# Optimization experiments

Measured on AMD Instinct MI355X. Metric: run time of the kernel, lower is better.

The kernel has to match this reference:

```python
import jax, jax.numpy as jnp
import numpy as np

SAME_RANGE = 1.0  # forward() default same_range
FLOW_SCALE = 32.0  # realistic pixel displacements


def setup_inputs() -> dict:
    key = jax.random.key(0)
    k1, k2, k3 = jax.random.split(key, 3)
    H, W, C = 2160, 3840, 3
    img = jax.random.uniform(k1, (H, W, C), dtype=jnp.float32)
    flow = jax.random.normal(k2, (H, W, 2), dtype=jnp.float32) * FLOW_SCALE
    depth = jax.random.uniform(k3, (H, W), dtype=jnp.float32) * 100.0 + 0.1
    return {"img": img, "flow": flow, "depth": depth}


def reference(img, flow, depth):
    """Forward warping with depth z-buffer occlusion resolution.

    Each source pixel (y,x) is scattered to p1 = p0 + flow (clamped to the
    image). At each target cell, only the contributions whose depth is within
    SAME_RANGE of the minimum arriving depth survive; surviving contributions
    are averaged. Empty cells stay zero (matches np.zeros_like init in the
    original C-library warp).
    """
    H, W, C = img.shape
    N = H * W
    gy, gx = jnp.meshgrid(jnp.arange(H, dtype=flow.dtype),
                          jnp.arange(W, dtype=flow.dtype), indexing='ij')
    # safe_x / safe_y clamped target coordinates
    tx = jnp.clip(gx + flow[..., 0], 0.0, W - 1)
    ty = jnp.clip(gy + flow[..., 1], 0.0, H - 1)
    ix = jnp.round(tx).astype(jnp.int32)
    iy = jnp.round(ty).astype(jnp.int32)
    idx = jax.lax.stop_gradient((iy * W + ix).reshape(N))  # [N] flat targets

    d = depth.reshape(N)
    # z-buffer: min depth landing at each target cell
    zmin = jnp.full((N,), jnp.inf, dtype=d.dtype).at[idx].min(d)
    keep = (d <= zmin[idx] + SAME_RANGE).astype(img.dtype)  # [N]

    src = img.reshape(N, C) * keep[:, None]
    num = jnp.zeros((N, C), dtype=img.dtype).at[idx].add(src)
    cnt = jnp.zeros((N,), dtype=img.dtype).at[idx].add(keep)
    out = jnp.where(cnt[:, None] > 0, num / jnp.maximum(cnt, 1.0)[:, None], 0.0)
    return out.reshape(H, W, C)
```

## Files before the change

### kernel.cpp

```cpp
#include <hip/hip_runtime.h>

#define HH 2160
#define WW 3840
#define NN (HH * WW)

#define SROWS 2
#define NSTRIP (HH / SROWS)
#define CPS (SROWS * WW)

#define BTH 256
#define GRP 2
#define GPX 4
#define PXB (BTH * GRP * GPX)

#define WIN 192

#define CSTRIDE 16

#define ICAP 12288
#define ECAP 262144
#define E0BASE ((u32)NSTRIP * ICAP)
#define E1BASE (E0BASE + ECAP)
#define TOTAL_RECS ((size_t)E1BASE + ECAP)

typedef unsigned long long u64;
typedef unsigned int u32;
typedef float f4n __attribute__((ext_vector_type(4)));

__device__ __forceinline__ u32 strip_base(int s) {
    if (s == 0) return E0BASE;
    if (s == NSTRIP - 1) return E1BASE;
    return (u32)s * ICAP;
}


__global__ __launch_bounds__(256) void init_cursor_kernel(u32* __restrict__ cursor)
{
    int s = blockIdx.x * blockDim.x + threadIdx.x;
    if (s < NSTRIP) cursor[(size_t)s * CSTRIDE] = strip_base(s);
}

__global__ __launch_bounds__(BTH, 6) void scatter_kernel(
    const float4* __restrict__ img4,
    const float4* __restrict__ flow4,
    const float4* __restrict__ depth4,
    u32* __restrict__ cursor,
    u64* __restrict__ recs)
{
    __shared__ u32 lc[WIN];
    __shared__ u32 gb[WIN];

    const int t = threadIdx.x;
    if (t < WIN) lc[t] = 0;
    __syncthreads();

    const int wb = blockIdx.x * PXB;
    const int ywb = wb / WW;
    int w0 = (ywb >> 1) - (WIN / 2);
    w0 = w0 < 0 ? 0 : (w0 > NSTRIP - WIN ? NSTRIP - WIN : w0);

    const int p0 = wb + t * GPX;
    const int p1 = wb + BTH * GPX + t * GPX;

    float4 fa0 = flow4[(p0 >> 1) + 0], fb0 = flow4[(p0 >> 1) + 1];
    float4 fa1 = flow4[(p1 >> 1) + 0], fb1 = flow4[(p1 >> 1) + 1];
    float4 dv0 = depth4[p0 >> 2];
    float4 dv1 = depth4[p1 >> 2];
    int ib0 = (p0 * 3) >> 2, ib1 = (p1 * 3) >> 2;
    float4 a0 = img4[ib0 + 0], a1 = img4[ib0 + 1], a2 = img4[ib0 + 2];
    float4 c0 = img4[ib1 + 0], c1 = img4[ib1 + 1], c2 = img4[ib1 + 2];

    u64 rrec[GRP][GPX];
    u32 aux[GRP][GPX];

    #pragma unroll
    for (int g = 0; g < GRP; ++g) {
        int p = g ? p1 : p0;
        int y = p / WW;
        int x = p - y * WW;
        float4 fa = g ? fa1 : fa0, fb = g ? fb1 : fb0;
        float4 dv = g ? dv1 : dv0;
        float4 i0 = g ? c0 : a0, i1 = g ? c1 : a1, i2 = g ? c2 : a2;
        float fx[GPX] = { fa.x, fa.z, fb.x, fb.z };
        float fy[GPX] = { fa.y, fa.w, fb.y, fb.w };
        float rr[GPX] = { i0.x, i0.w, i1.z, i2.y };
        float gg[GPX] = { i0.y, i1.x, i1.w, i2.z };
        float bb[GPX] = { i0.z, i1.y, i2.x, i2.w };
        float dd[GPX] = { dv.x, dv.y, dv.z, dv.w };
        #pragma unroll
        for (int k = 0; k < GPX; ++k) {
            float tx = fminf(fmaxf((float)(x + k) + fx[k], 0.0f), (float)(WW - 1));
            float ty = fminf(fmaxf((float)y + fy[k], 0.0f), (float)(HH - 1));
            int ix = (int)rintf(tx);
            int iy = (int)rintf(ty);
            int st = iy >> 1;
            u32 cell = (u32)((iy & 1) * WW + ix);
            u32 rq = (u32)(rr[k] * 63.0f + 0.5f);
            u32 gq = (u32)(gg[k] * 127.0f + 0.5f);
            u32 bq = (u32)(bb[k] * 63.0f + 0.5f);
            u64 rec = ((u64)__float_as_uint(dd[k]) << 32)
                    | ((u64)cell << 19)
                    | (u64)(rq | (gq << 6) | (bq << 13));
            rrec[g][k] = rec;
            int wst = st - w0;
            if ((unsigned)wst < WIN) {
                u32 rank = atomicAdd(&lc[wst], 1u);
                aux[g][k] = ((u32)wst << 13) | rank;
            } else {
                u32 slot = atomicAdd(&cursor[(size_t)st * CSTRIDE], 1u);
                recs[slot] = rec;
                aux[g][k] = 0xFFFFFFFFu;
            }
        }
    }
    __syncthreads();

    if (t < WIN) {
        u32 c = lc[t];
        if (c) gb[t] = atomicAdd(&cursor[(size_t)(w0 + t) * CSTRIDE], c);
    }
    __syncthreads();

    #pragma unroll
    for (int g = 0; g < GRP; ++g) {
        #pragma unroll
        for (int k = 0; k < GPX; ++k) {
            u32 a = aux[g][k];
            if (a != 0xFFFFFFFFu) {
                u32 wst = a >> 13, rank = a & 8191u;
                recs[(size_t)gb[wst] + rank] = rrec[g][k];
            }
        }
    }
}

__global__ __launch_bounds__(1024) void strip_kernel(
    const u64* __restrict__ recs,
    const u32* __restrict__ cursor,
    float* __restrict__ out)
{
    __shared__ u32 zmin[CPS];
    __shared__ u64 acc[CPS];
    int t = threadIdx.x;
    for (int c = t; c < CPS; c += 1024) { zmin[c] = 0xFFFFFFFFu; acc[c] = 0ull; }
    __syncthreads();

    int bs = blockIdx.x;
    int s = (bs == 0) ? 0 : (bs == 1 ? (NSTRIP - 1) : bs - 1);
    u32 lo = strip_base(s);
    u32 n = cursor[(size_t)s * CSTRIDE] - lo;
    const ulonglong2* rp = (const ulonglong2*)(recs + lo);
    u32 npair = n >> 1;

    for (u32 j = t; j < npair; j += 1024) {
        ulonglong2 rr = rp[j];
        atomicMin(&zmin[(u32)(rr.x >> 19) & 8191u], (u32)(rr.x >> 32));
        atomicMin(&zmin[(u32)(rr.y >> 19) & 8191u], (u32)(rr.y >> 32));
    }
    if (t == 0 && (n & 1)) {
        u64 rec = recs[lo + n - 1];
        atomicMin(&zmin[(u32)(rec >> 19) & 8191u], (u32)(rec >> 32));
    }
    __syncthreads();

    for (u32 j = t; j < npair; j += 1024) {
        ulonglong2 rr = rp[j];
        #pragma unroll
        for (int h = 0; h < 2; ++h) {
            u64 rec = h ? rr.y : rr.x;
            u32 cell = (u32)(rec >> 19) & 8191u;
            float d = __uint_as_float((u32)(rec >> 32));
            float z = __uint_as_float(zmin[cell]);
            if (d <= z + 1.0f) {
                u64 a = 1ull
                      | (((u64)rec & 63ull) << 10)
                      | ((((u64)rec >> 6) & 127ull) << 26)
                      | ((((u64)rec >> 13) & 63ull) << 43);
                atomicAdd(&acc[cell], a);
            }
        }
    }
    if (t == 0 && (n & 1)) {
        u64 rec = recs[lo + n - 1];
        u32 cell = (u32)(rec >> 19) & 8191u;
        float d = __uint_as_float((u32)(rec >> 32));
        float z = __uint_as_float(zmin[cell]);
        if (d <= z + 1.0f) {
            u64 a = 1ull
                  | (((u64)rec & 63ull) << 10)
                  | ((((u64)rec >> 6) & 127ull) << 26)
                  | ((((u64)rec >> 13) & 63ull) << 43);
            atomicAdd(&acc[cell], a);
        }
    }
    __syncthreads();

    float* o = out + (size_t)s * CPS * 3;
    for (int c0 = t * 4; c0 < CPS; c0 += 1024 * 4) {
        float v[12];
        #pragma unroll
        for (int k = 0; k < 4; ++k) {
            u64 p = acc[c0 + k];
            u32 cnt = (u32)(p & 1023u);
            float r = 0.0f, g = 0.0f, b = 0.0f;
            if (cnt) {
                float invc = 1.0f / (float)cnt;
                r = (float)((p >> 10) & 0xFFFFull) * (invc * (1.0f / 63.0f));
                g = (float)((p >> 26) & 0x1FFFFull) * (invc * (1.0f / 127.0f));
                b = (float)((p >> 43) & 0xFFFFull) * (invc * (1.0f / 63.0f));
            }
            v[3 * k + 0] = r; v[3 * k + 1] = g; v[3 * k + 2] = b;
        }
        f4n* o4 = (f4n*)(o + 3 * c0);
        f4n w0v = { v[0], v[1], v[2],  v[3]  };
        f4n w1v = { v[4], v[5], v[6],  v[7]  };
        f4n w2v = { v[8], v[9], v[10], v[11] };
        __builtin_nontemporal_store(w0v, &o4[0]);
        __builtin_nontemporal_store(w1v, &o4[1]);
        __builtin_nontemporal_store(w2v, &o4[2]);
    }
}

__device__ __forceinline__ int target_idx(int i, const float2* __restrict__ flow) {
    int y = i / WW;
    int x = i - y * WW;
    float2 f = flow[i];
    float tx = fminf(fmaxf((float)x + f.x, 0.0f), (float)(WW - 1));
    float ty = fminf(fmaxf((float)y + f.y, 0.0f), (float)(HH - 1));
    return (int)rintf(ty) * WW + (int)rintf(tx);
}

__global__ __launch_bounds__(256) void scatter_min_kernel(
    const float2* __restrict__ flow,
    const float* __restrict__ depth,
    u32* __restrict__ zmin)
{
    int i = blockIdx.x * blockDim.x + threadIdx.x;
    if (i >= NN) return;
    int idx = target_idx(i, flow);
    u32 db = __float_as_uint(depth[i]);
    u32 cur = zmin[idx];
    if (db < cur) atomicMin(&zmin[idx], db);
}

__global__ __launch_bounds__(256) void scatter_add_packed_kernel(
    const float* __restrict__ img,
    const float2* __restrict__ flow,
    const float* __restrict__ depth,
    const u32* __restrict__ zmin,
    u64* __restrict__ acc)
{
    int i = blockIdx.x * blockDim.x + threadIdx.x;
    if (i >= NN) return;
    int idx = target_idx(i, flow);
    float d = depth[i];
    float z = __uint_as_float(zmin[idx]);
    if (d <= z + 1.0f) {
        u64 rq = (u64)(u32)(img[3 * i + 0] * 127.0f + 0.5f);
        u64 gq = (u64)(u32)(img[3 * i + 1] * 127.0f + 0.5f);
        u64 bq = (u64)(u32)(img[3 * i + 2] * 127.0f + 0.5f);
        atomicAdd(&acc[idx], (rq << 48) | (gq << 32) | (bq << 16) | 1ull);
    }
}

__global__ __launch_bounds__(256) void finalize_packed_kernel(
    const u64* __restrict__ acc,
    float* __restrict__ out)
{
    int i = blockIdx.x * blockDim.x + threadIdx.x;
    if (i >= NN) return;
    u64 p = acc[i];
    u32 cnt = (u32)(p & 0xFFFFull);
    float r = 0.0f, g = 0.0f, b = 0.0f;
    if (cnt) {
        float inv = 1.0f / (127.0f * (float)cnt);
        r = (float)((p >> 48) & 0xFFFFull) * inv;
        g = (float)((p >> 32) & 0xFFFFull) * inv;
        b = (float)((p >> 16) & 0xFFFFull) * inv;
    }
    out[3 * i + 0] = r;
    out[3 * i + 1] = g;
    out[3 * i + 2] = b;
}

extern "C" void kernel_launch(void* const* d_in, const int* in_sizes, int n_in,
                              void* d_out, int out_size, void* d_ws, size_t ws_size,
                              hipStream_t stream)
{
    const float*  img   = (const float*)d_in[0];
    const float*  flow  = (const float*)d_in[1];
    const float*  depth = (const float*)d_in[2];
    float* out = (float*)d_out;

    const size_t rec_bytes = TOTAL_RECS * 8;
    const size_t cur_off   = (rec_bytes + 255) & ~(size_t)255;
    const size_t cur_bytes = (size_t)NSTRIP * CSTRIDE * sizeof(u32);

    if (ws_size >= cur_off + cur_bytes) {
        u64* recs   = (u64*)d_ws;
        u32* cursor = (u32*)((char*)d_ws + cur_off);

        init_cursor_kernel<<<(NSTRIP + 255) / 256, 256, 0, stream>>>(cursor);

        const int nwg = NN / PXB;
        scatter_kernel<<<nwg, BTH, 0, stream>>>(
            (const float4*)img, (const float4*)flow, (const float4*)depth,
            cursor, recs);
        strip_kernel<<<NSTRIP, 1024, 0, stream>>>(recs, cursor, out);
    } else {
        const size_t zb = (size_t)NN * 4;
        u32* zmin = (u32*)d_ws;
        u64* acc  = (u64*)((char*)d_ws + zb);

        hipMemsetAsync(zmin, 0xFF, zb, stream);
        hipMemsetAsync(acc, 0, (size_t)NN * 8, stream);

        const int block = 256;
        const int grid = (NN + block - 1) / block;
        scatter_min_kernel<<<grid, block, 0, stream>>>((const float2*)flow, depth, zmin);
        scatter_add_packed_kernel<<<grid, block, 0, stream>>>(img, (const float2*)flow, depth, zmin, acc);
        finalize_packed_kernel<<<grid, block, 0, stream>>>(acc, out);
    }
}
```

Before: 134.2 us.

## Stage scatter inputs through LDS with coalesced loads and strided pixel ownership

```diff
diff --git a/kernel.cpp b/kernel.cpp
--- a/kernel.cpp
+++ b/kernel.cpp
@@ -9,12 +9,10 @@
 #define CPS (SROWS * WW)
 
 #define BTH 256
-#define GRP 2
-#define GPX 4
-#define PXB (BTH * GRP * GPX)
+#define PXT 4
+#define PXB (BTH * PXT)
 
 #define WIN 192
-
 #define CSTRIDE 16
 
 #define ICAP 12288
@@ -47,70 +45,73 @@
     u32* __restrict__ cursor,
     u64* __restrict__ recs)
 {
+    __shared__ float lsf[PXB * 2];
+    __shared__ float lsd[PXB];
+    __shared__ float lsi[PXB * 3];
     __shared__ u32 lc[WIN];
     __shared__ u32 gb[WIN];
 
     const int t = threadIdx.x;
     if (t < WIN) lc[t] = 0;
-    __syncthreads();
 
     const int wb = blockIdx.x * PXB;
+
+    float4 f0 = flow4[(wb >> 1) + t];
+    float4 f1 = flow4[(wb >> 1) + BTH + t];
+    float4 d0 = depth4[(wb >> 2) + t];
+    float4 i0 = img4[((wb >> 2) * 3) + t];
+    float4 i1 = img4[((wb >> 2) * 3) + BTH + t];
+    float4 i2 = img4[((wb >> 2) * 3) + 2 * BTH + t];
+
+    ((float4*)lsf)[t]           = f0;
+    ((float4*)lsf)[BTH + t]     = f1;
+    ((float4*)lsd)[t]           = d0;
+    ((float4*)lsi)[t]           = i0;
+    ((float4*)lsi)[BTH + t]     = i1;
+    ((float4*)lsi)[2 * BTH + t] = i2;
+    __syncthreads();
+
     const int ywb = wb / WW;
     int w0 = (ywb >> 1) - (WIN / 2);
     w0 = w0 < 0 ? 0 : (w0 > NSTRIP - WIN ? NSTRIP - WIN : w0);
 
-    const int p0 = wb + t * GPX;
-    const int p1 = wb + BTH * GPX + t * GPX;
-
-    float4 fa0 = flow4[(p0 >> 1) + 0], fb0 = flow4[(p0 >> 1) + 1];
-    float4 fa1 = flow4[(p1 >> 1) + 0], fb1 = flow4[(p1 >> 1) + 1];
-    float4 dv0 = depth4[p0 >> 2];
-    float4 dv1 = depth4[p1 >> 2];
-    int ib0 = (p0 * 3) >> 2, ib1 = (p1 * 3) >> 2;
-    float4 a0 = img4[ib0 + 0], a1 = img4[ib0 + 1], a2 = img4[ib0 + 2];
-    float4 c0 = img4[ib1 + 0], c1 = img4[ib1 + 1], c2 = img4[ib1 + 2];
-
-    u64 rrec[GRP][GPX];
-    u32 aux[GRP][GPX];
+    u64 rrec[PXT];
+    u32 aux[PXT];
 
     #pragma unroll
-    for (int g = 0; g < GRP; ++g) {
-        int p = g ? p1 : p0;
+    for (int k = 0; k < PXT; ++k) {
+        int pl = t + k * BTH;
+        int p  = wb + pl;
         int y = p / WW;
         int x = p - y * WW;
-        float4 fa = g ? fa1 : fa0, fb = g ? fb1 : fb0;
-        float4 dv = g ? dv1 : dv0;
-        float4 i0 = g ? c0 : a0, i1 = g ? c1 : a1, i2 = g ? c2 : a2;
-        float fx[GPX] = { fa.x, fa.z, fb.x, fb.z };
-        float fy[GPX] = { fa.y, fa.w, fb.y, fb.w };
-        float rr[GPX] = { i0.x, i0.w, i1.z, i2.y };
-        float gg[GPX] = { i0.y, i1.x, i1.w, i2.z };
-        float bb[GPX] = { i0.z, i1.y, i2.x, i2.w };
-        float dd[GPX] = { dv.x, dv.y, dv.z, dv.w };
-        #pragma unroll
-        for (int k = 0; k < GPX; ++k) {
-            float tx = fminf(fmaxf((float)(x + k) + fx[k], 0.0f), (float)(WW - 1));
-            float ty = fminf(fmaxf((float)y + fy[k], 0.0f), (float)(HH - 1));
-            int ix = (int)rintf(tx);
-            int iy = (int)rintf(ty);
-            int st = iy >> 1;
-            u32 cell = (u32)((iy & 1) * WW + ix);
-            u32 rq = (u32)(rr[k] * 63.0f + 0.5f);
-            u32 gq = (u32)(gg[k] * 127.0f + 0.5f);
-            u32 bq = (u32)(bb[k] * 63.0f + 0.5f);
-            u64 rec = ((u64)__float_as_uint(dd[k]) << 32)
-                    | ((u64)cell << 19)
-                    | (u64)(rq | (gq << 6) | (bq << 13));
-            rrec[g][k] = rec;
-            int wst = st - w0;
-            if ((unsigned)wst < WIN) {
-                u32 rank = atomicAdd(&lc[wst], 1u);
-                aux[g][k] = ((u32)wst << 13) | rank;
-            } else {
-                u32 slot = atomicAdd(&cursor[(size_t)st * CSTRIDE], 1u);
-                recs[slot] = rec;
-                aux[g][k] = 0xFFFFFFFFu;
-            }
+        float fx = lsf[2 * pl + 0];
+        float fy = lsf[2 * pl + 1];
+        float dd = lsd[pl];
+        float rr = lsi[3 * pl + 0];
+        float gg = lsi[3 * pl + 1];
+        float bb = lsi[3 * pl + 2];
+
+        float tx = fminf(fmaxf((float)x + fx, 0.0f), (float)(WW - 1));
+        float ty = fminf(fmaxf((float)y + fy, 0.0f), (float)(HH - 1));
+        int ix = (int)rintf(tx);
+        int iy = (int)rintf(ty);
+        int st = iy >> 1;
+        u32 cell = (u32)((iy & 1) * WW + ix);
+        u32 rq = (u32)(rr * 63.0f + 0.5f);
+        u32 gq = (u32)(gg * 127.0f + 0.5f);
+        u32 bq = (u32)(bb * 63.0f + 0.5f);
+        u64 rec = ((u64)__float_as_uint(dd) << 32)
+                | ((u64)cell << 19)
+                | (u64)(rq | (gq << 6) | (bq << 13));
+        rrec[k] = rec;
+        int wst = st - w0;
+        if ((unsigned)wst < WIN) {
+            u32 rank = atomicAdd(&lc[wst], 1u);
+            aux[k] = ((u32)wst << 13) | rank;
+        } else {
+            u32 slot = atomicAdd(&cursor[(size_t)st * CSTRIDE], 1u);
+            recs[slot] = rec;
+            aux[k] = 0xFFFFFFFFu;
         }
     }
     __syncthreads();
@@ -122,14 +123,11 @@
     __syncthreads();
 
     #pragma unroll
-    for (int g = 0; g < GRP; ++g) {
-        #pragma unroll
-        for (int k = 0; k < GPX; ++k) {
-            u32 a = aux[g][k];
-            if (a != 0xFFFFFFFFu) {
-                u32 wst = a >> 13, rank = a & 8191u;
-                recs[(size_t)gb[wst] + rank] = rrec[g][k];
-            }
+    for (int k = 0; k < PXT; ++k) {
+        u32 a = aux[k];
+        if (a != 0xFFFFFFFFu) {
+            u32 wst = a >> 13, rank = a & 8191u;
+            recs[(size_t)gb[wst] + rank] = rrec[k];
         }
     }
 }
```

Result: slower. 151.6 us (+13.0%).
